# Performance work log

Hardware: AMD Instinct MI355X
Metric: run time of the kernel (lower is better)

The kernel has to match this reference:

```python
import jax, jax.numpy as jnp
from jax import lax
import numpy as np

NDIM = 256
BATCH = 65536
NROT = NDIM * (NDIM - 1) // 2  # comb(ndim, 2) = 32640


def _givens_mat(rots, ii, jj, ndim):
    """Product G_last @ ... @ G_1 of Givens rotations in combinations order.

    Left-multiplying by G(i, j, theta) only modifies rows i and j, so we apply
    each rotation as a rank-2 row update instead of a full matmul (same math
    as the original `plane_rot_mat @ mat` loop).
    """
    def step(mat, carry):
        i, j, th = carry
        c = jnp.cos(th)
        s = jnp.sin(th)
        ri = mat[i]
        rj = mat[j]
        mat = mat.at[i].set(c * ri - s * rj)
        mat = mat.at[j].set(s * ri + c * rj)
        return mat, None

    mat0 = jnp.eye(ndim, dtype=jnp.complex64)
    mat, _ = lax.scan(step, mat0, (ii, jj, rots))
    return mat


def setup_inputs() -> dict:
    key = jax.random.key(0)
    k1, k2, k3, k4 = jax.random.split(key, 4)
    x = jax.random.normal(k1, (BATCH, NDIM), dtype=jnp.float32)
    rots1 = 0.1 * jax.random.normal(k2, (NROT,), dtype=jnp.float32)
    phases = 0.1 * jax.random.normal(k3, (NDIM,), dtype=jnp.float32)
    rots2 = 0.1 * jax.random.normal(k4, (NROT,), dtype=jnp.float32)
    return {"x": x, "rots1": rots1, "phases": phases, "rots2": rots2}


def reference(x, rots1, phases, rots2):
    ndim = x.shape[1]
    # np.triu_indices(ndim, 1) enumerates (i, j) pairs in the same row-major
    # order as itertools.combinations(range(ndim), 2).
    ii_np, jj_np = np.triu_indices(ndim, k=1)
    ii = jnp.asarray(ii_np, dtype=jnp.int32)
    jj = jnp.asarray(jj_np, dtype=jnp.int32)

    # vector_norm: row-wise L2 normalization
    xn = x / jnp.linalg.norm(x, axis=1, keepdims=True)
    xc = xn.astype(jnp.complex64)

    # rot1: y = x @ M1.T with M1 = G_last @ ... @ G_1
    M1 = _givens_mat(rots1, ii, jj, ndim)
    y = xc @ M1.T

    # phase_transforms: x @ diag(exp(i*phases)) == elementwise phase multiply
    y = y * jnp.exp(1j * phases)

    # rot2
    M2 = _givens_mat(rots2, ii, jj, ndim)
    y = y @ M2.T

    # measure: |.|^2
    return jnp.abs(y) ** 2
```

## Files before the change

### kernel.cpp

```cpp
#include <hip/hip_runtime.h>
#include <stdint.h>
#include <math.h>

#define NDIM 256
#define BATCH 65536
#define NROT 32640

typedef float  f32x4 __attribute__((ext_vector_type(4)));
typedef short  s16x8 __attribute__((ext_vector_type(8)));
typedef unsigned int u32x4 __attribute__((ext_vector_type(4)));
typedef unsigned int u32x2 __attribute__((ext_vector_type(2)));

static __device__ __forceinline__ unsigned short f2bf(float f) {
    unsigned int u = __float_as_uint(f);
    u += 0x7fffu + ((u >> 16) & 1u);
    return (unsigned short)(u >> 16);
}
static __device__ __forceinline__ float bf2f(unsigned short h) {
    return __uint_as_float(((unsigned)h) << 16);
}

static __device__ __forceinline__ void split4(f32x4 v, u32x2* hi, u32x2* lo) {
    unsigned short h[4], l[4];
    #pragma unroll
    for (int i = 0; i < 4; i++) {
        h[i] = f2bf(v[i]);
        l[i] = f2bf(v[i] - bf2f(h[i]));
    }
    *hi = (u32x2){ (unsigned)h[0] | ((unsigned)h[1] << 16),
                   (unsigned)h[2] | ((unsigned)h[3] << 16) };
    *lo = (u32x2){ (unsigned)l[0] | ((unsigned)l[1] << 16),
                   (unsigned)l[2] | ((unsigned)l[3] << 16) };
}
static __device__ __forceinline__ void split8(const float* v, u32x4* hi, u32x4* lo) {
    unsigned short h[8], l[8];
    #pragma unroll
    for (int i = 0; i < 8; i++) {
        h[i] = f2bf(v[i]);
        l[i] = f2bf(v[i] - bf2f(h[i]));
    }
    *hi = (u32x4){ (unsigned)h[0] | ((unsigned)h[1] << 16),
                   (unsigned)h[2] | ((unsigned)h[3] << 16),
                   (unsigned)h[4] | ((unsigned)h[5] << 16),
                   (unsigned)h[6] | ((unsigned)h[7] << 16) };
    *lo = (u32x4){ (unsigned)l[0] | ((unsigned)l[1] << 16),
                   (unsigned)l[2] | ((unsigned)l[3] << 16),
                   (unsigned)l[4] | ((unsigned)l[5] << 16),
                   (unsigned)l[6] | ((unsigned)l[7] << 16) };
}

static __device__ __forceinline__ int sweep_bound(int k, int pblk) {
    int target = k * (NROT / pblk);
    int best = 0, bd = 0x7fffffff;
    for (int i = 0; i <= 256; i += 4) {
        int pre = i * 255 - (i * (i - 1)) / 2;
        int d = pre - target; d = (d < 0) ? -d : d;
        if (d < bd) { bd = d; best = i; }
    }
    return best;
}

__global__ __launch_bounds__(256) void k_cs(const float* __restrict__ r1,
                                            const float* __restrict__ r2,
                                            float2* __restrict__ cs) {
    int i = blockIdx.x * 256 + threadIdx.x;
    float th = (i < NROT) ? r1[i] : r2[i - NROT];
    float sv, cv; sincosf(th, &sv, &cv);
    cs[i] = make_float2(cv, sv);
}

__global__ __launch_bounds__(256) void k_blocks(const float2* __restrict__ cs,
                                                float* __restrict__ bmats, int pblk,
                                                const float* __restrict__ xg,
                                                unsigned short* __restrict__ xbf,
                                                int do_xn) {
    __shared__ float colb[264 * 64];
    __shared__ float2 csb[256 * 4];
    __shared__ float2 tri[24 * 6];

    const int bid = blockIdx.x;
    const int wid = threadIdx.x >> 6;
    const int lane = threadIdx.x & 63;

    if (wid != 0) {
        if (!do_xn) return;
        const int W  = bid * 3 + (wid - 1);
        const int nW = (int)gridDim.x * 3;
        const int per = (BATCH + nW - 1) / nW;
        int r0 = W * per;
        int rend = r0 + per; if (rend > BATCH) rend = BATCH;
        for (int row = r0; row < rend; row += 2) {
            const bool has2 = (row + 1 < rend);
            f32x4 v0 = *(const f32x4*)&xg[(size_t)row * 256 + lane * 4];
            f32x4 v1 = has2 ? *(const f32x4*)&xg[(size_t)(row + 1) * 256 + lane * 4]
                            : v0;
            float s0 = v0[0] * v0[0] + v0[1] * v0[1] + v0[2] * v0[2] + v0[3] * v0[3];
            float s1 = v1[0] * v1[0] + v1[1] * v1[1] + v1[2] * v1[2] + v1[3] * v1[3];
            #pragma unroll
            for (int off = 32; off; off >>= 1) {
                s0 += __shfl_xor(s0, off, 64);
                s1 += __shfl_xor(s1, off, 64);
            }
            float sc0 = 1.0f / sqrtf(s0), sc1 = 1.0f / sqrtf(s1);
            {
                unsigned short h0 = f2bf(v0[0] * sc0), h1 = f2bf(v0[1] * sc0);
                unsigned short h2 = f2bf(v0[2] * sc0), h3 = f2bf(v0[3] * sc0);
                u32x2 pk = { (unsigned)h0 | ((unsigned)h1 << 16),
                             (unsigned)h2 | ((unsigned)h3 << 16) };
                *(u32x2*)&xbf[(size_t)row * 256 + lane * 4] = pk;
            }
            if (has2) {
                unsigned short h0 = f2bf(v1[0] * sc1), h1 = f2bf(v1[1] * sc1);
                unsigned short h2 = f2bf(v1[2] * sc1), h3 = f2bf(v1[3] * sc1);
                u32x2 pk = { (unsigned)h0 | ((unsigned)h1 << 16),
                             (unsigned)h2 | ((unsigned)h3 << 16) };
                *(u32x2*)&xbf[(size_t)(row + 1) * 256 + lane * 4] = pk;
            }
        }
        return;
    }

    const int t = lane;
    const int chunk = bid & 3;
    const int b = (bid >> 2) % pblk;
    const int set = (bid >> 2) / pblk;
    const int col0 = chunk * 64;
    const float2* cst = cs + (size_t)set * NROT;

    const int s0 = sweep_bound(b, pblk);
    const int s1 = sweep_bound(b + 1, pblk);
    const int ngroups = (s1 - s0) >> 2;

    {
        const f32x4 z = {0.f, 0.f, 0.f, 0.f};
        #pragma unroll 11
        for (int q = 0; q < 66; q++)
            *(f32x4*)&colb[(q * 64 + t) * 4] = z;
        colb[(col0 + t) * 64 + t] = 1.0f;
    }

    for (int k = t; k < ngroups * 6; k += 64) {
        int g = k / 6, q = k - g * 6;
        int a  = (q < 3) ? 0 : ((q < 5) ? 1 : 2);
        int bb = (q < 3) ? (q + 1) : ((q < 5) ? (q - 1) : 3);
        int m0 = s0 + g * 4;
        int m = m0 + a;
        int base = m * 255 - (m * (m - 1)) / 2;
        tri[k] = cst[base - m - 1 + m0 + bb];
    }

    float2 gv[16];
    {
        const int m0g = s0;
        int offg[4];
        #pragma unroll
        for (int a = 0; a < 4; a++) {
            int m = m0g + a;
            offg[a] = m * 255 - (m * (m - 1)) / 2 - m - 1;
        }
        #pragma unroll
        for (int it = 0; it < 16; it++) {
            int k = t + it * 64;
            int jj = k >> 2, a = k & 3;
            int j = m0g + 4 + jj;
            gv[it] = (j < 256) ? cst[offg[a] + j] : make_float2(1.f, 0.f);
        }
        #pragma unroll
        for (int it = 0; it < 16; it++)
            csb[t + it * 64] = gv[it];
    }

    for (int g = 0; g < ngroups; g++) {
        const int m0 = s0 + g * 4;
        const int n_j = 252 - m0;
        const int n_p = (n_j > 0) ? ((n_j + 7) & ~7) : 0;
        const float* csbuf = (const float*)&csb[0];

        const bool have_next = (g + 1 < ngroups);
        if (have_next) {
            const int m0g = m0 + 4;
            int offg[4];
            #pragma unroll
            for (int a = 0; a < 4; a++) {
                int m = m0g + a;
                offg[a] = m * 255 - (m * (m - 1)) / 2 - m - 1;
            }
            #pragma unroll
            for (int it = 0; it < 16; it++) {
                int k = t + it * 64;
                int jj = k >> 2, a = k & 3;
                int j = m0g + 4 + jj;
                gv[it] = (j < 256) ? cst[offg[a] + j] : make_float2(1.f, 0.f);
            }
        }

        float u0 = colb[(m0 + 0) * 64 + t];
        float u1 = colb[(m0 + 1) * 64 + t];
        float u2 = colb[(m0 + 2) * 64 + t];
        float u3 = colb[(m0 + 3) * 64 + t];

        {
            float2 cv; float nr;
            cv = tri[g * 6 + 0]; nr = cv.y * u0 + cv.x * u1; u0 = cv.x * u0 - cv.y * u1; u1 = nr;
            cv = tri[g * 6 + 1]; nr = cv.y * u0 + cv.x * u2; u0 = cv.x * u0 - cv.y * u2; u2 = nr;
            cv = tri[g * 6 + 2]; nr = cv.y * u0 + cv.x * u3; u0 = cv.x * u0 - cv.y * u3; u3 = nr;
            cv = tri[g * 6 + 3]; nr = cv.y * u1 + cv.x * u2; u1 = cv.x * u1 - cv.y * u2; u2 = nr;
            cv = tri[g * 6 + 4]; nr = cv.y * u1 + cv.x * u3; u1 = cv.x * u1 - cv.y * u3; u3 = nr;
            cv = tri[g * 6 + 5]; nr = cv.y * u2 + cv.x * u3; u2 = cv.x * u2 - cv.y * u3; u3 = nr;
        }

        if (n_p > 0) {
            float rbuf[8];
            f32x4 abuf[8][2];
            #pragma unroll
            for (int p = 0; p < 8; p++) {
                rbuf[p] = colb[(m0 + 4 + p) * 64 + t];
                abuf[p][0] = *(const f32x4*)&csbuf[p * 8 + 0];
                abuf[p][1] = *(const f32x4*)&csbuf[p * 8 + 4];
            }
            for (int c = 0; c < n_p; c += 8) {
                #pragma unroll
                for (int p = 0; p < 8; p++) {
                    const int j = m0 + 4 + c + p;
                    float r = rbuf[p];
                    f32x4 A01 = abuf[p][0], A23 = abuf[p][1];
                    int jn = j + 8; jn = (jn < 263) ? jn : 263;
                    int cn = c + p + 8; cn = (cn < n_p) ? cn : (n_p - 1);
                    rbuf[p] = colb[jn * 64 + t];
                    abuf[p][0] = *(const f32x4*)&csbuf[cn * 8 + 0];
                    abuf[p][1] = *(const f32x4*)&csbuf[cn * 8 + 4];
                    float nr;
                    nr = A01[1] * u0 + A01[0] * r; u0 = A01[0] * u0 - A01[1] * r; r = nr;
                    nr = A01[3] * u1 + A01[2] * r; u1 = A01[2] * u1 - A01[3] * r; r = nr;
                    nr = A23[1] * u2 + A23[0] * r; u2 = A23[0] * u2 - A23[1] * r; r = nr;
                    nr = A23[3] * u3 + A23[2] * r; u3 = A23[2] * u3 - A23[3] * r; r = nr;
                    colb[j * 64 + t] = r;
                }
            }
        }
        colb[(m0 + 0) * 64 + t] = u0;
        colb[(m0 + 1) * 64 + t] = u1;
        colb[(m0 + 2) * 64 + t] = u2;
        colb[(m0 + 3) * 64 + t] = u3;

        if (have_next) {
            #pragma unroll
            for (int it = 0; it < 16; it++)
                csb[t + it * 64] = gv[it];
        }
    }

    float* outm = bmats + (size_t)(set * pblk + b) * 65536;
    for (int r = 0; r < 256; r++)
        outm[(size_t)r * 256 + col0 + t] = colb[r * 64 + t];
}

#define TB 2560

static __device__ __forceinline__ int bslot(int row, int s) {
    return row * 40 + ((s ^ ((row >> 3) & 3)) << 3);
}

static __device__ __forceinline__ void tile_issueA(const float* __restrict__ Am,
                                                   int tr, int kb, int tid,
                                                   f32x4 va[2]) {
    #pragma unroll
    for (int it = 0; it < 2; it++) {
        int flat = tid + it * 256;
        int r = flat >> 3, c4 = flat & 7;
        va[it] = *(const f32x4*)&Am[(size_t)(tr * 64 + r) * 256 + kb * 32 + c4 * 4];
    }
}
static __device__ __forceinline__ void tile_issueB(const float* __restrict__ Bm,
                                                   int tc, int kb, int bn, int bkq,
                                                   float vb[8]) {
    #pragma unroll
    for (int i = 0; i < 8; i++)
        vb[i] = Bm[(size_t)(kb * 32 + bkq * 8 + i) * 256 + tc * 64 + bn];
}
static __device__ __forceinline__ void tile_commit(unsigned short* __restrict__ Ahi,
                                                   unsigned short* __restrict__ Alo,
                                                   unsigned short* __restrict__ Bhi,
                                                   unsigned short* __restrict__ Blo,
                                                   int tid, int bn, int bkq,
                                                   const f32x4 va[2], const float vb[8]) {
    #pragma unroll
    for (int it = 0; it < 2; it++) {
        int flat = tid + it * 256;
        int r = flat >> 3, c4 = flat & 7;
        u32x2 hi, lo; split4(va[it], &hi, &lo);
        *(u32x2*)&Ahi[r * 40 + c4 * 4] = hi;
        *(u32x2*)&Alo[r * 40 + c4 * 4] = lo;
    }
    u32x4 hi8, lo8; split8(vb, &hi8, &lo8);
    *(u32x4*)&Bhi[bslot(bn, bkq)] = hi8;
    *(u32x4*)&Blo[bslot(bn, bkq)] = lo8;
}
static __device__ __forceinline__ void tile_mfma(const unsigned short* __restrict__ Ahi,
                                                 const unsigned short* __restrict__ Alo,
                                                 const unsigned short* __restrict__ Bhi,
                                                 const unsigned short* __restrict__ Blo,
                                                 int mh, int nh, int l15, int lq,
                                                 f32x4 acc[2][2]) {
    s16x8 ah[2], al[2], bh[2], bl[2];
    #pragma unroll
    for (int tm = 0; tm < 2; tm++) {
        ah[tm] = *(const s16x8*)&Ahi[(mh + tm * 16 + l15) * 40 + lq * 8];
        al[tm] = *(const s16x8*)&Alo[(mh + tm * 16 + l15) * 40 + lq * 8];
    }
    #pragma unroll
    for (int tn = 0; tn < 2; tn++) {
        bh[tn] = *(const s16x8*)&Bhi[bslot(nh + tn * 16 + l15, lq)];
        bl[tn] = *(const s16x8*)&Blo[bslot(nh + tn * 16 + l15, lq)];
    }
    #pragma unroll
    for (int tm = 0; tm < 2; tm++)
        #pragma unroll
        for (int tn = 0; tn < 2; tn++) {
            acc[tm][tn] = __builtin_amdgcn_mfma_f32_16x16x32_bf16(ah[tm], bh[tn], acc[tm][tn], 0, 0, 0);
            acc[tm][tn] = __builtin_amdgcn_mfma_f32_16x16x32_bf16(ah[tm], bl[tn], acc[tm][tn], 0, 0, 0);
            acc[tm][tn] = __builtin_amdgcn_mfma_f32_16x16x32_bf16(al[tm], bh[tn], acc[tm][tn], 0, 0, 0);
        }
}

static __device__ void combine_tile(const float* __restrict__ src,
                                    float* __restrict__ dst,
                                    int half, int pblk, int bx, int by, int tid,
                                    unsigned short* Ahi, unsigned short* Alo,
                                    unsigned short* Bhi, unsigned short* Blo) {
    const int set = by / half, pidx = by % half;
    const int stride = pblk / (2 * half);
    const int s0A = sweep_bound((2 * pidx + 1) * stride, pblk);
    const float* Am = src + (size_t)(set * 2 * half + 2 * pidx + 1) * 65536;
    const float* Bm = src + (size_t)(set * 2 * half + 2 * pidx) * 65536;
    float* Dm = dst + (size_t)(set * half + pidx) * 65536;
    const int tr = bx >> 2, tc = bx & 3;

    if (tr * 64 + 64 <= s0A) {
        #pragma unroll
        for (int it = 0; it < 4; it++) {
            int flat = tid + it * 256;
            int r = flat >> 4, c4 = flat & 15;
            size_t idx = (size_t)(tr * 64 + r) * 256 + tc * 64 + c4 * 4;
            *(f32x4*)&Dm[idx] = *(const f32x4*)&Bm[idx];
        }
        return;
    }
    const int kb0 = (tr * 64 >= s0A) ? (s0A >> 5) : 0;

    const int lane = tid & 63, w = tid >> 6;
    const int mh = (w >> 1) * 32, nh = (w & 1) * 32;
    const int l15 = lane & 15, lq = lane >> 4;
    const int bn = tid & 63, bkq = tid >> 6;

    f32x4 acc[2][2];
    #pragma unroll
    for (int i = 0; i < 2; i++)
        #pragma unroll
        for (int j = 0; j < 2; j++) acc[i][j] = (f32x4){0.f, 0.f, 0.f, 0.f};

    f32x4 vaE[2], vaO[2]; float vbE[8], vbO[8];
    tile_issueA(Am, tr, kb0, tid, vaE);
    tile_issueB(Bm, tc, kb0, bn, bkq, vbE);
    if (kb0 + 1 < 8) {
        tile_issueA(Am, tr, kb0 + 1, tid, vaO);
        tile_issueB(Bm, tc, kb0 + 1, bn, bkq, vbO);
    }

    for (int kb = kb0; kb < 8; kb++) {
        const int cur = (kb - kb0) & 1;
        if (cur == 0) {
            tile_commit(Ahi, Alo, Bhi, Blo, tid, bn, bkq, vaE, vbE);
            __syncthreads();
            if (kb + 2 < 8) {
                tile_issueA(Am, tr, kb + 2, tid, vaE);
                tile_issueB(Bm, tc, kb + 2, bn, bkq, vbE);
            }
        } else {
            tile_commit(Ahi, Alo, Bhi, Blo, tid, bn, bkq, vaO, vbO);
            __syncthreads();
            if (kb + 2 < 8) {
                tile_issueA(Am, tr, kb + 2, tid, vaO);
                tile_issueB(Bm, tc, kb + 2, bn, bkq, vbO);
            }
        }
        tile_mfma(Ahi, Alo, Bhi, Blo, mh, nh, l15, lq, acc);
        __syncthreads();
    }
    #pragma unroll
    for (int tm = 0; tm < 2; tm++)
        #pragma unroll
        for (int tn = 0; tn < 2; tn++)
            #pragma unroll
            for (int r = 0; r < 4; r++)
                Dm[(size_t)(tr * 64 + mh + tm * 16 + lq * 4 + r) * 256
                   + tc * 64 + nh + tn * 16 + l15] = acc[tm][tn][r];
}

__global__ __launch_bounds__(256) void k_combine(const float* __restrict__ src,
                                                 float* __restrict__ dst,
                                                 int half, int pblk) {
    __shared__ unsigned short Ahi[TB], Alo[TB], Bhi[TB], Blo[TB];
    combine_tile(src, dst, half, pblk, blockIdx.x, blockIdx.y, threadIdx.x,
                 Ahi, Alo, Bhi, Blo);
}

__global__ __launch_bounds__(256) void k_abt_part(const float* __restrict__ mats,
                                                  const float* __restrict__ phases,
                                                  float* __restrict__ part) {
    __shared__ unsigned short Ahi[TB], Alo[TB], Bhi[TB], Blo[TB];
    const float* Am = mats + 65536;
    const float* Bm = mats;
    const int tid = threadIdx.x;
    const int bx = blockIdx.x;
    const int v  = blockIdx.y;
    const int kb = blockIdx.z;
    const int tr = bx >> 2, tc = bx & 3;

    const int lane = tid & 63, w = tid >> 6;
    const int mh = (w >> 1) * 32, nh = (w & 1) * 32;
    const int l15 = lane & 15, lq = lane >> 4;
    const int bn = tid & 63, bkq = tid >> 6;

    f32x4 va[2]; float vb[8];
    tile_issueA(Am, tr, kb, tid, va);
    #pragma unroll
    for (int i = 0; i < 8; i++) {
        int kg = kb * 32 + bkq * 8 + i;
        float ph = phases[kg];
        float sc = v ? sinf(ph) : cosf(ph);
        vb[i] = Bm[(size_t)kg * 256 + tc * 64 + bn] * sc;
    }

    f32x4 acc[2][2];
    #pragma unroll
    for (int i = 0; i < 2; i++)
        #pragma unroll
        for (int j = 0; j < 2; j++) acc[i][j] = (f32x4){0.f, 0.f, 0.f, 0.f};

    tile_commit(Ahi, Alo, Bhi, Blo, tid, bn, bkq, va, vb);
    __syncthreads();
    tile_mfma(Ahi, Alo, Bhi, Blo, mh, nh, l15, lq, acc);

    float* pp = part + (size_t)(kb * 2 + v) * 65536;
    #pragma unroll
    for (int tm = 0; tm < 2; tm++)
        #pragma unroll
        for (int tn = 0; tn < 2; tn++)
            #pragma unroll
            for (int r = 0; r < 4; r++)
                pp[(size_t)(tr * 64 + mh + tm * 16 + lq * 4 + r) * 256
                   + tc * 64 + nh + tn * 16 + l15] = acc[tm][tn][r];
}

__global__ __launch_bounds__(256) void k_abt_red(const float* __restrict__ part,
                                                 unsigned short* __restrict__ abt) {
    const int e = (blockIdx.x * 256 + threadIdx.x) * 4;
    f32x4 s = {0.f, 0.f, 0.f, 0.f};
    #pragma unroll
    for (int kz = 0; kz < 8; kz++)
        s += *(const f32x4*)&part[(size_t)kz * 131072 + e];
    unsigned short h0 = f2bf(s[0]), h1 = f2bf(s[1]);
    unsigned short h2 = f2bf(s[2]), h3 = f2bf(s[3]);
    u32x2 pk = { (unsigned)h0 | ((unsigned)h1 << 16),
                 (unsigned)h2 | ((unsigned)h3 << 16) };
    *(u32x2*)&abt[e] = pk;
}

__global__ __launch_bounds__(256) void k_norm(const float* __restrict__ x,
                                              float* __restrict__ invn) {
    const int row = blockIdx.x * 4 + (threadIdx.x >> 6);
    const int lane = threadIdx.x & 63;
    f32x4 v = *(const f32x4*)&x[(size_t)row * 256 + lane * 4];
    float s = v[0] * v[0] + v[1] * v[1] + v[2] * v[2] + v[3] * v[3];
    for (int off = 32; off; off >>= 1) s += __shfl_xor(s, off, 64);
    if (lane == 0) invn[row] = 1.0f / sqrtf(s);
}

#define BKP 136
__global__ __launch_bounds__(256) void k_gemm_bf(const unsigned short* __restrict__ xbf,
                                                 const unsigned short* __restrict__ abt,
                                                 float* __restrict__ out) {
    __shared__ unsigned short As[128 * BKP];
    __shared__ unsigned short Bs[128 * BKP];
    const int tid = threadIdx.x;
    const int l  = blockIdx.y * 4 + blockIdx.x;
    const int L  = (l & 7) * 256 + (l >> 3);
    const int cb = L & 3;
    const int rb = L >> 2;
    const int lane = tid & 63, w = tid >> 6;

    f32x4 acc[16];
    #pragma unroll
    for (int i = 0; i < 16; i++) acc[i] = (f32x4){0.f, 0.f, 0.f, 0.f};

    int rA[8], cA[8], grB[8];
    #pragma unroll
    for (int it = 0; it < 8; it++) {
        int flat = tid + it * 256;
        rA[it] = flat >> 4; cA[it] = flat & 15;
        int r = rA[it];
        grB[it] = (r < 64) ? (cb * 64 + r) : (256 + cb * 64 + (r - 64));
    }

    u32x4 pa[8], pb[8];
    #pragma unroll
    for (int it = 0; it < 8; it++) {
        pa[it] = *(const u32x4*)&xbf[(size_t)(rb * 128 + rA[it]) * 256 + cA[it] * 8];
        pb[it] = *(const u32x4*)&abt[(size_t)grB[it] * 256 + cA[it] * 8];
    }
    #pragma unroll
    for (int it = 0; it < 8; it++) {
        *(u32x4*)&As[rA[it] * BKP + cA[it] * 8] = pa[it];
        *(u32x4*)&Bs[rA[it] * BKP + cA[it] * 8] = pb[it];
    }
    __syncthreads();
    #pragma unroll
    for (int it = 0; it < 8; it++) {
        pa[it] = *(const u32x4*)&xbf[(size_t)(rb * 128 + rA[it]) * 256 + 128 + cA[it] * 8];
        pb[it] = *(const u32x4*)&abt[(size_t)grB[it] * 256 + 128 + cA[it] * 8];
    }

    auto compute = [&]() {
        #pragma unroll
        for (int ks = 0; ks < 4; ks++) {
            const int k0 = ks * 32 + (lane >> 4) * 8;
            s16x8 a[2], b[8];
            #pragma unroll
            for (int tm = 0; tm < 2; tm++)
                a[tm] = *(const s16x8*)&As[(w * 32 + tm * 16 + (lane & 15)) * BKP + k0];
            #pragma unroll
            for (int tn = 0; tn < 8; tn++)
                b[tn] = *(const s16x8*)&Bs[(tn * 16 + (lane & 15)) * BKP + k0];
            #pragma unroll
            for (int tm = 0; tm < 2; tm++)
                #pragma unroll
                for (int tn = 0; tn < 8; tn++)
                    acc[tm * 8 + tn] = __builtin_amdgcn_mfma_f32_16x16x32_bf16(
                        a[tm], b[tn], acc[tm * 8 + tn], 0, 0, 0);
        }
    };
    compute();
    __syncthreads();
    #pragma unroll
    for (int it = 0; it < 8; it++) {
        *(u32x4*)&As[rA[it] * BKP + cA[it] * 8] = pa[it];
        *(u32x4*)&Bs[rA[it] * BKP + cA[it] * 8] = pb[it];
    }
    __syncthreads();
    compute();

    const int qr = lane >> 4, c = lane & 15;
    #pragma unroll
    for (int tm = 0; tm < 2; tm++) {
        #pragma unroll
        for (int tn = 0; tn < 4; tn++) {
            f32x4 p = acc[tm * 8 + tn];
            f32x4 q = acc[tm * 8 + tn + 4];
            #pragma unroll
            for (int r = 0; r < 4; r++) {
                int m = w * 32 + tm * 16 + qr * 4 + r;
                out[(size_t)(rb * 128 + m) * 256 + cb * 64 + tn * 16 + c] =
                    p[r] * p[r] + q[r] * q[r];
            }
        }
    }
}

__global__ __launch_bounds__(256) void k_gemm_f32(const float* __restrict__ x,
                                                  const unsigned short* __restrict__ abt,
                                                  const float* __restrict__ invn,
                                                  float* __restrict__ out) {
    __shared__ unsigned short As[128 * BKP];
    __shared__ unsigned short Bs[128 * BKP];
    const int tid = threadIdx.x;
    const int l  = blockIdx.y * 4 + blockIdx.x;
    const int L  = (l & 7) * 256 + (l >> 3);
    const int cb = L & 3;
    const int rb = L >> 2;
    const int lane = tid & 63, w = tid >> 6;

    f32x4 acc[16];
    #pragma unroll
    for (int i = 0; i < 16; i++) acc[i] = (f32x4){0.f, 0.f, 0.f, 0.f};

    for (int kb = 0; kb < 2; kb++) {
        __syncthreads();
        #pragma unroll
        for (int it = 0; it < 16; it++) {
            int flat = tid + it * 256;
            int r = flat >> 5, c4 = flat & 31;
            f32x4 v = *(const f32x4*)&x[(size_t)(rb * 128 + r) * 256 + kb * 128 + c4 * 4];
            float sc = invn[rb * 128 + r];
            v[0] *= sc; v[1] *= sc; v[2] *= sc; v[3] *= sc;
            unsigned short h0 = f2bf(v[0]), h1 = f2bf(v[1]);
            unsigned short h2 = f2bf(v[2]), h3 = f2bf(v[3]);
            u32x2 pk = { (unsigned)h0 | ((unsigned)h1 << 16),
                         (unsigned)h2 | ((unsigned)h3 << 16) };
            *(u32x2*)&As[r * BKP + c4 * 4] = pk;
        }
        #pragma unroll
        for (int it = 0; it < 8; it++) {
            int flat = tid + it * 256;
            int r = flat >> 4, c8 = flat & 15;
            int gr = (r < 64) ? (cb * 64 + r) : (256 + cb * 64 + (r - 64));
            u32x4 vv = *(const u32x4*)&abt[(size_t)gr * 256 + kb * 128 + c8 * 8];
            *(u32x4*)&Bs[r * BKP + c8 * 8] = vv;
        }
        __syncthreads();
        #pragma unroll
        for (int ks = 0; ks < 4; ks++) {
            const int k0 = ks * 32 + (lane >> 4) * 8;
            s16x8 a[2], b[8];
            #pragma unroll
            for (int tm = 0; tm < 2; tm++)
                a[tm] = *(const s16x8*)&As[(w * 32 + tm * 16 + (lane & 15)) * BKP + k0];
            #pragma unroll
            for (int tn = 0; tn < 8; tn++)
                b[tn] = *(const s16x8*)&Bs[(tn * 16 + (lane & 15)) * BKP + k0];
            #pragma unroll
            for (int tm = 0; tm < 2; tm++)
                #pragma unroll
                for (int tn = 0; tn < 8; tn++)
                    acc[tm * 8 + tn] = __builtin_amdgcn_mfma_f32_16x16x32_bf16(
                        a[tm], b[tn], acc[tm * 8 + tn], 0, 0, 0);
        }
    }

    const int qr = lane >> 4, c = lane & 15;
    #pragma unroll
    for (int tm = 0; tm < 2; tm++) {
        #pragma unroll
        for (int tn = 0; tn < 4; tn++) {
            f32x4 p = acc[tm * 8 + tn];
            f32x4 q = acc[tm * 8 + tn + 4];
            #pragma unroll
            for (int r = 0; r < 4; r++) {
                int m = w * 32 + tm * 16 + qr * 4 + r;
                out[(size_t)(rb * 128 + m) * 256 + cb * 64 + tn * 16 + c] =
                    p[r] * p[r] + q[r] * q[r];
            }
        }
    }
}

extern "C" void kernel_launch(void* const* d_in, const int* in_sizes, int n_in,
                              void* d_out, int out_size, void* d_ws, size_t ws_size,
                              hipStream_t stream) {
    (void)in_sizes; (void)n_in; (void)out_size;
    const float* x      = (const float*)d_in[0];
    const float* rots1  = (const float*)d_in[1];
    const float* phases = (const float*)d_in[2];
    const float* rots2  = (const float*)d_in[3];
    float* out = (float*)d_out;
    char* ws = (char*)d_ws;

    const size_t MAT = 262144;
    int pblk = 64;
    while (pblk > 16 &&
           (size_t)3 * pblk * MAT + 2 * MAT + (size_t)BATCH * 512 > ws_size)
        pblk >>= 1;
    const size_t offA   = 0;
    const size_t offB   = offA + (size_t)2 * pblk * MAT;
    const size_t offABT = offB + (size_t)pblk * MAT;
    const size_t offINV = offABT + MAT;
    const size_t offXBF = offINV + MAT;
    const bool use_xbf = (offXBF + (size_t)BATCH * 512) <= ws_size;

    float*          A    = (float*)(ws + offA);
    float*          B    = (float*)(ws + offB);
    unsigned short* abt  = (unsigned short*)(ws + offABT);
    float*          invn = (float*)(ws + offINV);
    unsigned short* xbf  = (unsigned short*)(ws + offXBF);
    float2*         cs   = (float2*)(ws + offB);

    k_cs<<<(2 * NROT) / 256, 256, 0, stream>>>(rots1, rots2, cs);
    k_blocks<<<8 * pblk, 256, 0, stream>>>(cs, A, pblk, x, xbf, use_xbf ? 1 : 0);

    float* srcp = A; float* dstp = B;
    for (int half = pblk / 2; half >= 1; half >>= 1) {
        k_combine<<<dim3(16, 2 * half), 256, 0, stream>>>(srcp, dstp, half, pblk);
        float* tmp = srcp; srcp = dstp; dstp = tmp;
    }
    k_abt_part<<<dim3(16, 2, 8), 256, 0, stream>>>(srcp, phases, dstp);
    k_abt_red<<<128, 256, 0, stream>>>(dstp, abt);

    if (use_xbf) {
        k_gemm_bf<<<dim3(4, BATCH / 128), 256, 0, stream>>>(xbf, abt, out);
    } else {
        k_norm<<<BATCH / 4, 256, 0, stream>>>(x, invn);
        k_gemm_f32<<<dim3(4, BATCH / 128), 256, 0, stream>>>(x, abt, invn, out);
    }
}
```

Baseline: 261.5 us.

## Split-K the small late combine stages and halve the Givens block count

For the tree-combine levels with few matrix pairs (half < 8), the product is split along K into 8 partial tiles computed in parallel, then summed by a separate reduction kernel. Tiles and K-blocks known to be identity or zero are skipped. The output buffer serves as scratch for the partials. The initial block count pblk drops from 64 to 32, which shortens the tree but makes each k_blocks block apply more rotations. This trades extra launches and partial-sum traffic for better GPU occupancy in the serial tail of the reduction tree.

```diff
diff --git a/kernel.cpp b/kernel.cpp
--- a/kernel.cpp
+++ b/kernel.cpp
@@ -405,6 +405,77 @@
                  Ahi, Alo, Bhi, Blo);
 }
 
+__global__ __launch_bounds__(256) void k_combine_part(const float* __restrict__ src,
+                                                      float* __restrict__ part,
+                                                      int half, int pblk) {
+    __shared__ unsigned short Ahi[TB], Alo[TB], Bhi[TB], Blo[TB];
+    const int tid = threadIdx.x;
+    const int bx = blockIdx.x, by = blockIdx.y, kb = blockIdx.z;
+    const int set = by / half, pidx = by % half;
+    const int stride = pblk / (2 * half);
+    const int s0A = sweep_bound((2 * pidx + 1) * stride, pblk);
+    const float* Am = src + (size_t)(set * 2 * half + 2 * pidx + 1) * 65536;
+    const float* Bm = src + (size_t)(set * 2 * half + 2 * pidx) * 65536;
+    const int tr = bx >> 2, tc = bx & 3;
+
+    if (tr * 64 + 64 <= s0A) return;
+    const int kb0 = (tr * 64 >= s0A) ? (s0A >> 5) : 0;
+    if (kb < kb0) return;
+
+    const int lane = tid & 63, w = tid >> 6;
+    const int mh = (w >> 1) * 32, nh = (w & 1) * 32;
+    const int l15 = lane & 15, lq = lane >> 4;
+    const int bn = tid & 63, bkq = tid >> 6;
+
+    f32x4 va[2]; float vb[8];
+    tile_issueA(Am, tr, kb, tid, va);
+    tile_issueB(Bm, tc, kb, bn, bkq, vb);
+
+    f32x4 acc[2][2];
+    #pragma unroll
+    for (int i = 0; i < 2; i++)
+        #pragma unroll
+        for (int j = 0; j < 2; j++) acc[i][j] = (f32x4){0.f, 0.f, 0.f, 0.f};
+
+    tile_commit(Ahi, Alo, Bhi, Blo, tid, bn, bkq, va, vb);
+    __syncthreads();
+    tile_mfma(Ahi, Alo, Bhi, Blo, mh, nh, l15, lq, acc);
+
+    float* pp = part + (size_t)(by * 8 + kb) * 65536;
+    #pragma unroll
+    for (int tm = 0; tm < 2; tm++)
+        #pragma unroll
+        for (int tn = 0; tn < 2; tn++)
+            #pragma unroll
+            for (int r = 0; r < 4; r++)
+                pp[(size_t)(tr * 64 + mh + tm * 16 + lq * 4 + r) * 256
+                   + tc * 64 + nh + tn * 16 + l15] = acc[tm][tn][r];
+}
+
+__global__ __launch_bounds__(256) void k_combine_red(const float* __restrict__ src,
+                                                     const float* __restrict__ part,
+                                                     float* __restrict__ dst,
+                                                     int half, int pblk) {
+    const int idx = (blockIdx.x * 256 + threadIdx.x) * 4;
+    const int by = idx >> 16;
+    const int e  = idx & 65535;
+    const int set = by / half, pidx = by % half;
+    const int stride = pblk / (2 * half);
+    const int s0A = sweep_bound((2 * pidx + 1) * stride, pblk);
+    float* Dm = dst + (size_t)(set * half + pidx) * 65536;
+    const int band = e >> 14;
+    if (band * 64 + 64 <= s0A) {
+        const float* Bm = src + (size_t)(set * 2 * half + 2 * pidx) * 65536;
+        *(f32x4*)&Dm[e] = *(const f32x4*)&Bm[e];
+        return;
+    }
+    const int kb0 = (band * 64 >= s0A) ? (s0A >> 5) : 0;
+    f32x4 s = {0.f, 0.f, 0.f, 0.f};
+    for (int kb = kb0; kb < 8; kb++)
+        s += *(const f32x4*)&part[(size_t)(by * 8 + kb) * 65536 + e];
+    *(f32x4*)&Dm[e] = s;
+}
+
 __global__ __launch_bounds__(256) void k_abt_part(const float* __restrict__ mats,
                                                   const float* __restrict__ phases,
                                                   float* __restrict__ part) {
@@ -656,7 +727,7 @@
     char* ws = (char*)d_ws;
 
     const size_t MAT = 262144;
-    int pblk = 64;
+    int pblk = 32;
     while (pblk > 16 &&
            (size_t)3 * pblk * MAT + 2 * MAT + (size_t)BATCH * 512 > ws_size)
         pblk >>= 1;
@@ -673,13 +744,21 @@
     float*          invn = (float*)(ws + offINV);
     unsigned short* xbf  = (unsigned short*)(ws + offXBF);
     float2*         cs   = (float2*)(ws + offB);
+    float*          scr  = out;
 
     k_cs<<<(2 * NROT) / 256, 256, 0, stream>>>(rots1, rots2, cs);
     k_blocks<<<8 * pblk, 256, 0, stream>>>(cs, A, pblk, x, xbf, use_xbf ? 1 : 0);
 
     float* srcp = A; float* dstp = B;
     for (int half = pblk / 2; half >= 1; half >>= 1) {
-        k_combine<<<dim3(16, 2 * half), 256, 0, stream>>>(srcp, dstp, half, pblk);
+        if (half >= 8) {
+            k_combine<<<dim3(16, 2 * half), 256, 0, stream>>>(srcp, dstp, half, pblk);
+        } else {
+            k_combine_part<<<dim3(16, 2 * half, 8), 256, 0, stream>>>(srcp, scr,
+                                                                      half, pblk);
+            k_combine_red<<<128 * half, 256, 0, stream>>>(srcp, scr, dstp,
+                                                          half, pblk);
+        }
         float* tmp = srcp; srcp = dstp; dstp = tmp;
     }
     k_abt_part<<<dim3(16, 2, 8), 256, 0, stream>>>(srcp, phases, dstp);
```

Result: slower. 273.3 us (+4.5%).
